# Performance work log

Hardware: AMD Instinct MI355X
Metric: run time of the kernel (lower is better)

The kernel has to match this reference:

```python
import jax, jax.numpy as jnp
import numpy as np

B, U, F = 32768, 256, 256  # batch, units, input features
LR = 0.01                  # inner_lr
EPS = 1e-3                 # TF LayerNormalization default epsilon


def _layer_norm(x, gamma, beta):
    m = jnp.mean(x, axis=-1, keepdims=True)
    v = jnp.var(x, axis=-1, keepdims=True)
    return (x - m) * jax.lax.rsqrt(v + EPS) * gamma + beta


def _enc(W1, b1, W2, b2, u):
    # mlp_2 inner encoder: Dense(4U, gelu-exact) -> Dense(U)
    return jax.nn.gelu(u @ W1 + b1, approximate=False) @ W2 + b2


def setup_inputs() -> dict:
    key = jax.random.key(0)
    ks = jax.random.split(key, 12)
    def w(k, shape):
        fan_in = shape[0]
        return jax.random.normal(k, shape, jnp.float32) / np.sqrt(fan_in)
    return {
        "x": jax.random.normal(ks[0], (B, F), jnp.float32),
        "h_prev": jax.random.normal(ks[1], (B, U), jnp.float32),
        "W_phi": w(ks[2], (F + U, U)), "b_phi": jnp.zeros((U,), jnp.float32),
        "W_psi": w(ks[3], (F + U, U)), "b_psi": jnp.zeros((U,), jnp.float32),
        "W1": w(ks[4], (U, 4 * U)), "b1": jnp.zeros((4 * U,), jnp.float32),
        "W2": w(ks[5], (4 * U, U)), "b2": jnp.zeros((U,), jnp.float32),
        "W_g": w(ks[6], (U, U)), "g_bias": jnp.zeros((U,), jnp.float32),
        "ln_gamma": jnp.ones((U,), jnp.float32), "ln_beta": jnp.zeros((U,), jnp.float32),
        "W_h": w(ks[7], (U, U)), "h_bias": jnp.zeros((U,), jnp.float32),
    }


def reference(x, h_prev, W_phi, b_phi, W_psi, b_psi, W1, b1, W2, b2,
              W_g, g_bias, ln_gamma, ln_beta, W_h, h_bias):
    z = jnp.concatenate([x, h_prev], axis=-1)          # [B, F+U]
    phi = z @ W_phi + b_phi                            # [B, U], also the inner target

    def inner_loss(params):
        W1_, b1_, W2_, b2_ = params
        r = _enc(W1_, b1_, W2_, b2_, phi) @ W_g + g_bias
        r = _layer_norm(r, ln_gamma, ln_beta)
        return jnp.mean(jnp.square(r - phi)), r

    params = (W1, b1, W2, b2)
    # inner_iterations = 1: one SGD step on the inner-encoder weights only
    (_, recon), grads = jax.value_and_grad(inner_loss, has_aux=True)(params)
    params = tuple(p - LR * g for p, g in zip(params, grads))

    psi = z @ W_psi + b_psi                            # [B, U]
    feat = _enc(*params, psi) + 0.1 * recon            # updated encoder on psi
    out = feat @ W_h + h_bias                          # new hidden / cell output
    return out
```

## Files before the change

### kernel.cpp

```cpp
#include <hip/hip_runtime.h>
#include <math.h>

#define B_N 32768
#define U_N 256
#define H_N 1024
#define LR_C 0.01f
#define EPS_C 1e-3f

typedef unsigned short ushort_t;
typedef unsigned int uint_t;
using frag8 = __attribute__((ext_vector_type(8))) short;
using f32x4 = __attribute__((ext_vector_type(4))) float;

__device__ __forceinline__ float erf_fast(float y) {
    float ay = fabsf(y);
    float t = __builtin_amdgcn_rcpf(fmaf(0.3275911f, ay, 1.0f));
    float p = fmaf(1.061405429f, t, -1.453152027f);
    p = fmaf(p, t, 1.421413741f);
    p = fmaf(p, t, -0.284496736f);
    p = fmaf(p, t, 0.254829592f);
    p = p * t;
    float e = __expf(-ay * ay);
    float r = fmaf(-p, e, 1.0f);
    return copysignf(r, y);
}
__device__ __forceinline__ float gelu_f(float x) {
    return 0.5f * x * (1.0f + erf_fast(x * 0.7071067811865475f));
}
__device__ __forceinline__ void gelu_pair(float x, float& g, float& d) {
    float ay = fabsf(x) * 0.7071067811865475f;
    float t = __builtin_amdgcn_rcpf(fmaf(0.3275911f, ay, 1.0f));
    float p = fmaf(1.061405429f, t, -1.453152027f);
    p = fmaf(p, t, 1.421413741f);
    p = fmaf(p, t, -0.284496736f);
    p = fmaf(p, t, 0.254829592f);
    p = p * t;
    float e = __expf(-ay * ay);
    float er = copysignf(fmaf(-p, e, 1.0f), x);
    float c = 0.5f * (1.0f + er);
    g = x * c;
    d = fmaf(x * 0.3989422804014327f, e, c);
}
__device__ __forceinline__ void splitf(float v, ushort_t& h, ushort_t& l) {
    uint_t u = __float_as_uint(v);
    h = (ushort_t)(u >> 16);
    float r = v - __uint_as_float(u & 0xFFFF0000u);
    uint_t ru = __float_as_uint(r);
    l = (ushort_t)((ru + 0x7FFFu + ((ru >> 16) & 1u)) >> 16);
}
__device__ __forceinline__ ushort_t cvt_rne(float v) {
    uint_t u = __float_as_uint(v);
    return (ushort_t)((u + 0x7FFFu + ((u >> 16) & 1u)) >> 16);
}
__device__ __forceinline__ float bf2f(ushort_t u) {
    return __uint_as_float((uint_t)u << 16);
}
__device__ __forceinline__ void unpack2(uint_t pa, uint_t pb, uint_t& hw, uint_t& lw) {
    hw = __builtin_amdgcn_perm(pb, pa, 0x07060302u);
    lw = __builtin_amdgcn_perm(pb, pa, 0x05040100u);
}
__device__ __forceinline__ size_t swz(int n, int k, int K) {
    return (size_t)n * K +
           (size_t)((k & ~31) | ((((k >> 3) & 3) ^ ((n >> 1) & 3)) << 3) | (k & 7));
}
__device__ __forceinline__ void gload16(const ushort_t* g, ushort_t* l) {
    __builtin_amdgcn_global_load_lds(
        (const __attribute__((address_space(1))) void*)g,
        (__attribute__((address_space(3))) void*)l, 16, 0, 0);
}

#define EPI_NONE 0
#define EPI_GELU 1
#define EPI_ADDS 3

#define BEP_P   0
#define BEP_PT  1
#define BEP_A1  2
#define BEP_DAT 3

template<int ACONCAT, int APACK, int EPI, int OPACK>
__global__ __launch_bounds__(256)
void mgemm_k(const float* A, const float* A2, const uint_t* __restrict__ AP,
             const ushort_t* __restrict__ BTh, const ushort_t* __restrict__ BTl,
             const float* __restrict__ bias, const ushort_t* __restrict__ Xr,
             float* C, uint_t* Cp,
             int M, int N, int K)
{
    __shared__ ushort_t Ah[128 * 40], Al[128 * 40];
    __shared__ ushort_t Bh[128 * 32], Bl[128 * 32];
    const int tid = threadIdx.x;
    const int m0 = blockIdx.x * 128, n0 = blockIdx.y * 128;
    const int lane = tid & 63, w = tid >> 6;
    const int wm = (w & 1) * 64, wn = (w >> 1) * 64;
    const int fr = lane & 15, fq = lane >> 4;
    const int sr = tid >> 1;
    const int sk = (tid & 1) * 16;

    f32x4 acc[4][4];
    #pragma unroll
    for (int i = 0; i < 4; i++)
        #pragma unroll
        for (int j = 0; j < 4; j++) acc[i][j] = (f32x4){0.f, 0.f, 0.f, 0.f};

    for (int k0 = 0; k0 < K; k0 += 32) {
        {
            const int r0w = w * 32;
            const size_t so = (size_t)(n0 + r0w + (lane >> 2)) * K + k0 + ((lane & 3) << 3);
            gload16(&BTh[so],                  &Bh[r0w * 32]);
            gload16(&BTh[so + (size_t)16 * K], &Bh[(r0w + 16) * 32]);
            gload16(&BTl[so],                  &Bl[r0w * 32]);
            gload16(&BTl[so + (size_t)16 * K], &Bl[(r0w + 16) * 32]);
        }
        if (APACK) {
            const uint_t* ap = AP + (size_t)(m0 + sr) * K + k0 + sk;
            uint4 p0 = *(const uint4*)(ap);
            uint4 p1 = *(const uint4*)(ap + 4);
            uint4 p2 = *(const uint4*)(ap + 8);
            uint4 p3 = *(const uint4*)(ap + 12);
            uint4 h0, h1, l0, l1;
            unpack2(p0.x, p0.y, h0.x, l0.x); unpack2(p0.z, p0.w, h0.y, l0.y);
            unpack2(p1.x, p1.y, h0.z, l0.z); unpack2(p1.z, p1.w, h0.w, l0.w);
            unpack2(p2.x, p2.y, h1.x, l1.x); unpack2(p2.z, p2.w, h1.y, l1.y);
            unpack2(p3.x, p3.y, h1.z, l1.z); unpack2(p3.z, p3.w, h1.w, l1.w);
            *(uint4*)&Ah[sr * 40 + sk]     = h0;
            *(uint4*)&Ah[sr * 40 + sk + 8] = h1;
            *(uint4*)&Al[sr * 40 + sk]     = l0;
            *(uint4*)&Al[sr * 40 + sk + 8] = l1;
        } else {
            #pragma unroll
            for (int g = 0; g < 2; g++) {
                uint4 qh, qa;
                uint_t ph[4], pl[4];
                #pragma unroll
                for (int c = 0; c < 2; c++) {
                    const int ak = k0 + sk + g * 8 + c * 4;
                    const float* ap;
                    if (ACONCAT) ap = (ak < 256) ? (A + (size_t)(m0 + sr) * 256 + ak)
                                                 : (A2 + (size_t)(m0 + sr) * 256 + (ak - 256));
                    else         ap = A + (size_t)(m0 + sr) * K + ak;
                    float4 v = *(const float4*)ap;
                    ushort_t h0,h1,h2,h3,l0,l1,l2,l3;
                    splitf(v.x,h0,l0); splitf(v.y,h1,l1); splitf(v.z,h2,l2); splitf(v.w,h3,l3);
                    ph[c*2]   = (uint_t)h0 | ((uint_t)h1 << 16);
                    ph[c*2+1] = (uint_t)h2 | ((uint_t)h3 << 16);
                    pl[c*2]   = (uint_t)l0 | ((uint_t)l1 << 16);
                    pl[c*2+1] = (uint_t)l2 | ((uint_t)l3 << 16);
                }
                qh.x = ph[0]; qh.y = ph[1]; qh.z = ph[2]; qh.w = ph[3];
                qa.x = pl[0]; qa.y = pl[1]; qa.z = pl[2]; qa.w = pl[3];
                *(uint4*)&Ah[sr * 40 + sk + g * 8] = qh;
                *(uint4*)&Al[sr * 40 + sk + g * 8] = qa;
            }
        }
        __syncthreads();

        frag8 afh[4], afl[4], bfh[4], bfl[4];
        #pragma unroll
        for (int i = 0; i < 4; i++) {
            const int ar = wm + i * 16 + fr;
            afh[i] = *(frag8*)&Ah[ar * 40 + fq * 8];
            afl[i] = *(frag8*)&Al[ar * 40 + fq * 8];
        }
        #pragma unroll
        for (int j = 0; j < 4; j++) {
            const int br = wn + j * 16 + fr;
            const int bs = br * 32 + ((fq ^ ((br >> 1) & 3)) << 3);
            bfh[j] = *(frag8*)&Bh[bs];
            bfl[j] = *(frag8*)&Bl[bs];
        }
        #pragma unroll
        for (int i = 0; i < 4; i++)
            #pragma unroll
            for (int j = 0; j < 4; j++) {
                acc[i][j] = __builtin_amdgcn_mfma_f32_16x16x32_bf16(afh[i], bfh[j], acc[i][j], 0, 0, 0);
                acc[i][j] = __builtin_amdgcn_mfma_f32_16x16x32_bf16(afh[i], bfl[j], acc[i][j], 0, 0, 0);
                acc[i][j] = __builtin_amdgcn_mfma_f32_16x16x32_bf16(afl[i], bfh[j], acc[i][j], 0, 0, 0);
            }
        __syncthreads();
    }

    float bv[4] = {0.f, 0.f, 0.f, 0.f};
    if (bias != nullptr)
        #pragma unroll
        for (int j = 0; j < 4; j++) bv[j] = bias[n0 + wn + j * 16 + fr];
    #pragma unroll
    for (int i = 0; i < 4; i++)
        #pragma unroll
        for (int j = 0; j < 4; j++) {
            const int col = n0 + wn + j * 16 + fr;
            #pragma unroll
            for (int r = 0; r < 4; r++) {
                const int row = m0 + wm + i * 16 + fq * 4 + r;
                const size_t off = (size_t)row * N + col;
                float c = acc[i][j][r] + bv[j];
                if (EPI == EPI_GELU)      c = gelu_f(c);
                else if (EPI == EPI_ADDS) c = c + 0.1f * bf2f(Xr[off]);
                if (OPACK) {
                    ushort_t h, l;
                    splitf(c, h, l);
                    Cp[off] = ((uint_t)h << 16) | (uint_t)l;
                } else {
                    C[off] = c;
                }
            }
        }
}

template<int ACONCAT, int BEP>
__global__ __launch_bounds__(256)
void bgemm_k(const void* Av, const float* A2f, const ushort_t* __restrict__ BTh,
             const float* __restrict__ bias, const ushort_t* __restrict__ GpIn,
             ushort_t* Crm, ushort_t* Cct, ushort_t* GpOut,
             int M, int N, int K)
{
    __shared__ ushort_t Ah[128 * 40];
    __shared__ ushort_t Bh[128 * 32];
    const int tid = threadIdx.x;
    const int m0 = blockIdx.x * 128, n0 = blockIdx.y * 128;
    const int lane = tid & 63, w = tid >> 6;
    const int wm = (w & 1) * 64, wn = (w >> 1) * 64;
    const int fr = lane & 15, fq = lane >> 4;
    const int sr = tid >> 1;
    const int sk = (tid & 1) * 16;

    f32x4 acc[4][4];
    #pragma unroll
    for (int i = 0; i < 4; i++)
        #pragma unroll
        for (int j = 0; j < 4; j++) acc[i][j] = (f32x4){0.f, 0.f, 0.f, 0.f};

    for (int k0 = 0; k0 < K; k0 += 32) {
        {
            const int r0w = w * 32;
            const size_t so = (size_t)(n0 + r0w + (lane >> 2)) * K + k0 + ((lane & 3) << 3);
            gload16(&BTh[so],                  &Bh[r0w * 32]);
            gload16(&BTh[so + (size_t)16 * K], &Bh[(r0w + 16) * 32]);
        }
        if (ACONCAT) {
            const float* A = (const float*)Av;
            #pragma unroll
            for (int g = 0; g < 2; g++) {
                uint_t ph[4];
                #pragma unroll
                for (int c = 0; c < 2; c++) {
                    const int ak = k0 + sk + g * 8 + c * 4;
                    const float* ap = (ak < 256) ? (A + (size_t)(m0 + sr) * 256 + ak)
                                                 : (A2f + (size_t)(m0 + sr) * 256 + (ak - 256));
                    float4 v = *(const float4*)ap;
                    ph[c*2]   = (uint_t)cvt_rne(v.x) | ((uint_t)cvt_rne(v.y) << 16);
                    ph[c*2+1] = (uint_t)cvt_rne(v.z) | ((uint_t)cvt_rne(v.w) << 16);
                }
                uint4 q; q.x = ph[0]; q.y = ph[1]; q.z = ph[2]; q.w = ph[3];
                *(uint4*)&Ah[sr * 40 + sk + g * 8] = q;
            }
        } else {
            const ushort_t* A = (const ushort_t*)Av;
            const size_t ao = (size_t)(m0 + sr) * K + k0 + sk;
            *(uint4*)&Ah[sr * 40 + sk]     = *(const uint4*)&A[ao];
            *(uint4*)&Ah[sr * 40 + sk + 8] = *(const uint4*)&A[ao + 8];
        }
        __syncthreads();

        frag8 af[4], bf[4];
        #pragma unroll
        for (int i = 0; i < 4; i++) af[i] = *(frag8*)&Ah[(wm + i * 16 + fr) * 40 + fq * 8];
        #pragma unroll
        for (int j = 0; j < 4; j++) {
            const int br = wn + j * 16 + fr;
            bf[j] = *(frag8*)&Bh[br * 32 + ((fq ^ ((br >> 1) & 3)) << 3)];
        }
        #pragma unroll
        for (int i = 0; i < 4; i++)
            #pragma unroll
            for (int j = 0; j < 4; j++)
                acc[i][j] = __builtin_amdgcn_mfma_f32_16x16x32_bf16(af[i], bf[j], acc[i][j], 0, 0, 0);
        __syncthreads();
    }

    float bv[4] = {0.f, 0.f, 0.f, 0.f};
    if (bias != nullptr)
        #pragma unroll
        for (int j = 0; j < 4; j++) bv[j] = bias[n0 + wn + j * 16 + fr];
    #pragma unroll
    for (int i = 0; i < 4; i++)
        #pragma unroll
        for (int j = 0; j < 4; j++) {
            const int col = n0 + wn + j * 16 + fr;
            const int rowb = m0 + wm + i * 16 + fq * 4;
            float v[4];
            #pragma unroll
            for (int r = 0; r < 4; r++) v[r] = acc[i][j][r] + bv[j];
            if (BEP == BEP_A1) {
                ushort_t gc[4];
                #pragma unroll
                for (int r = 0; r < 4; r++) {
                    float g, d;
                    gelu_pair(v[r], g, d);
                    gc[r] = cvt_rne(g);
                    Crm[(size_t)(rowb + r) * N + col] = gc[r];
                    GpOut[(size_t)(rowb + r) * N + col] = cvt_rne(d);
                }
                uint_t p0 = (uint_t)gc[0] | ((uint_t)gc[1] << 16);
                uint_t p1 = (uint_t)gc[2] | ((uint_t)gc[3] << 16);
                *(uint2*)&Cct[(size_t)col * M + rowb] = (uint2){p0, p1};
            } else if (BEP == BEP_DAT) {
                ushort_t dc[4];
                #pragma unroll
                for (int r = 0; r < 4; r++)
                    dc[r] = cvt_rne(v[r] * bf2f(GpIn[(size_t)(rowb + r) * N + col]));
                uint_t p0 = (uint_t)dc[0] | ((uint_t)dc[1] << 16);
                uint_t p1 = (uint_t)dc[2] | ((uint_t)dc[3] << 16);
                *(uint2*)&Cct[(size_t)col * M + rowb] = (uint2){p0, p1};
            } else {
                ushort_t cc[4];
                #pragma unroll
                for (int r = 0; r < 4; r++) {
                    cc[r] = cvt_rne(v[r]);
                    Crm[(size_t)(rowb + r) * N + col] = cc[r];
                }
                if (BEP == BEP_PT) {
                    uint_t p0 = (uint_t)cc[0] | ((uint_t)cc[1] << 16);
                    uint_t p1 = (uint_t)cc[2] | ((uint_t)cc[3] << 16);
                    *(uint2*)&Cct[(size_t)col * M + rowb] = (uint2){p0, p1};
                }
            }
        }
}

__global__ __launch_bounds__(256)
void wgrad_k(const ushort_t* __restrict__ AT, const ushort_t* __restrict__ BTt,
             float* C, int M, int N, int KA, int kofsA, int KB, int kofsB, int KC)
{
    __shared__ ushort_t Ah[128 * 40];
    __shared__ ushort_t Bh[128 * 40];
    const int tid = threadIdx.x;
    const int m0 = blockIdx.x * 128, n0 = blockIdx.y * 128;
    const int kbA = kofsA + blockIdx.z * KC;
    const int kbB = kofsB + blockIdx.z * KC;
    const int lane = tid & 63, w = tid >> 6;
    const int wm = (w & 1) * 64, wn = (w >> 1) * 64;
    const int fr = lane & 15, fq = lane >> 4;
    const int sr = tid >> 1;
    const int sk = (tid & 1) * 16;

    f32x4 acc[4][4];
    #pragma unroll
    for (int i = 0; i < 4; i++)
        #pragma unroll
        for (int j = 0; j < 4; j++) acc[i][j] = (f32x4){0.f, 0.f, 0.f, 0.f};

    for (int k0 = 0; k0 < KC; k0 += 32) {
        const size_t ao = (size_t)(m0 + sr) * KA + kbA + k0 + sk;
        *(uint4*)&Ah[sr * 40 + sk]     = *(const uint4*)&AT[ao];
        *(uint4*)&Ah[sr * 40 + sk + 8] = *(const uint4*)&AT[ao + 8];
        const size_t bo = (size_t)(n0 + sr) * KB + kbB + k0 + sk;
        *(uint4*)&Bh[sr * 40 + sk]     = *(const uint4*)&BTt[bo];
        *(uint4*)&Bh[sr * 40 + sk + 8] = *(const uint4*)&BTt[bo + 8];
        __syncthreads();

        frag8 af[4], bf[4];
        #pragma unroll
        for (int i = 0; i < 4; i++) af[i] = *(frag8*)&Ah[(wm + i * 16 + fr) * 40 + fq * 8];
        #pragma unroll
        for (int j = 0; j < 4; j++) bf[j] = *(frag8*)&Bh[(wn + j * 16 + fr) * 40 + fq * 8];
        #pragma unroll
        for (int i = 0; i < 4; i++)
            #pragma unroll
            for (int j = 0; j < 4; j++)
                acc[i][j] = __builtin_amdgcn_mfma_f32_16x16x32_bf16(af[i], bf[j], acc[i][j], 0, 0, 0);
        __syncthreads();
    }
    #pragma unroll
    for (int i = 0; i < 4; i++)
        #pragma unroll
        for (int j = 0; j < 4; j++) {
            const int col = n0 + wn + j * 16 + fr;
            #pragma unroll
            for (int r = 0; r < 4; r++) {
                const int row = m0 + wm + i * 16 + fq * 4 + r;
                atomicAdd(&C[(size_t)row * N + col], acc[i][j][r]);
            }
        }
}

__global__ __launch_bounds__(256)
void colsumT_k(const ushort_t* __restrict__ T, float* db, int LD, int cols)
{
    const int n = blockIdx.x * 4 + (threadIdx.x >> 6);
    const int lane = threadIdx.x & 63;
    const ushort_t* row = T + (size_t)n * LD;
    float s = 0.f;
    for (int c = lane * 8; c < cols; c += 512) {
        uint4 q = *(const uint4*)&row[c];
        uint_t u[4] = {q.x, q.y, q.z, q.w};
        #pragma unroll
        for (int t = 0; t < 4; t++) {
            s += bf2f((ushort_t)(u[t] & 0xFFFF));
            s += bf2f((ushort_t)(u[t] >> 16));
        }
    }
    #pragma unroll
    for (int o = 32; o > 0; o >>= 1) s += __shfl_xor(s, o);
    if (lane == 0) atomicAdd(&db[n], s);
}

__global__ __launch_bounds__(256)
void ln_bf_k(const ushort_t* r0, const ushort_t* __restrict__ phi,
             const float* __restrict__ gamma, const float* __restrict__ beta,
             ushort_t* recon, ushort_t* dr0)
{
    const int lane = threadIdx.x & 63;
    const int wv = threadIdx.x >> 6;
    const int row = blockIdx.x * 4 + wv;
    const size_t base = (size_t)row * U_N + (lane << 2);

    uint2 xu = *(const uint2*)(r0 + base);
    uint2 pu = *(const uint2*)(phi + base);
    float xs[4] = { bf2f((ushort_t)(xu.x & 0xFFFF)), bf2f((ushort_t)(xu.x >> 16)),
                    bf2f((ushort_t)(xu.y & 0xFFFF)), bf2f((ushort_t)(xu.y >> 16)) };
    float ps[4] = { bf2f((ushort_t)(pu.x & 0xFFFF)), bf2f((ushort_t)(pu.x >> 16)),
                    bf2f((ushort_t)(pu.y & 0xFFFF)), bf2f((ushort_t)(pu.y >> 16)) };
    float s = xs[0] + xs[1] + xs[2] + xs[3];
    float sq = xs[0]*xs[0] + xs[1]*xs[1] + xs[2]*xs[2] + xs[3]*xs[3];
    #pragma unroll
    for (int o = 32; o > 0; o >>= 1) { s += __shfl_xor(s, o); sq += __shfl_xor(sq, o); }
    const float m   = s * (1.0f / U_N);
    const float var = sq * (1.0f / U_N) - m * m;
    const float inv = rsqrtf(var + EPS_C);

    float4 gv = *(const float4*)(gamma + (lane << 2));
    float4 bvv = *(const float4*)(beta + (lane << 2));
    float gs[4] = {gv.x, gv.y, gv.z, gv.w};
    float bs[4] = {bvv.x, bvv.y, bvv.z, bvv.w};
    float rh[4], dh[4], rc[4];
    float s1 = 0.f, s2 = 0.f;
    const float gscale = 2.0f / ((float)B_N * (float)U_N);
    #pragma unroll
    for (int j = 0; j < 4; j++) {
        rh[j] = (xs[j] - m) * inv;
        rc[j] = rh[j] * gs[j] + bs[j];
        float g2 = gscale * (rc[j] - ps[j]);
        dh[j] = g2 * gs[j];
        s1 += dh[j];
        s2 += dh[j] * rh[j];
    }
    #pragma unroll
    for (int o = 32; o > 0; o >>= 1) { s1 += __shfl_xor(s1, o); s2 += __shfl_xor(s2, o); }
    const float mu1 = s1 * (1.0f / U_N);
    const float mu2 = s2 * (1.0f / U_N);
    ushort_t oc[4], dc[4];
    #pragma unroll
    for (int j = 0; j < 4; j++) {
        oc[j] = cvt_rne(rc[j]);
        dc[j] = cvt_rne(inv * (dh[j] - mu1 - rh[j] * mu2));
    }
    *(uint2*)(recon + base) = (uint2){ (uint_t)oc[0] | ((uint_t)oc[1] << 16),
                                       (uint_t)oc[2] | ((uint_t)oc[3] << 16) };
    *(uint2*)(dr0 + base)   = (uint2){ (uint_t)dc[0] | ((uint_t)dc[1] << 16),
                                       (uint_t)dc[2] | ((uint_t)dc[3] << 16) };
}

template<int HASL>
__global__ __launch_bounds__(256)
void tsplit_k(const float* __restrict__ W, ushort_t* __restrict__ Th,
              ushort_t* __restrict__ Tl, int R, int C)
{
    __shared__ float t[64][65];
    const int tid = threadIdx.x;
    const int R0 = blockIdx.x * 64, C0 = blockIdx.y * 64;
    const int c = tid & 63, rb = (tid >> 6) * 16;
    for (int i = 0; i < 16; i++)
        t[rb + i][c] = W[(size_t)(R0 + rb + i) * C + C0 + c];
    __syncthreads();
    const int orr = tid & 63, ob = (tid >> 6) * 16;
    for (int i = 0; i < 16; i++) {
        const int oc = ob + i;
        ushort_t h, l;
        splitf(t[orr][oc], h, l);
        const size_t d = swz(C0 + oc, R0 + orr, R);
        Th[d] = h;
        if (HASL) Tl[d] = l;
    }
}

__global__ __launch_bounds__(256)
void tupd_k(const float* __restrict__ W, const float* __restrict__ dW,
            ushort_t* __restrict__ Th, ushort_t* __restrict__ Tl, int R, int C)
{
    __shared__ float t[64][65];
    const int tid = threadIdx.x;
    const int R0 = blockIdx.x * 64, C0 = blockIdx.y * 64;
    const int c = tid & 63, rb = (tid >> 6) * 16;
    for (int i = 0; i < 16; i++) {
        const size_t o = (size_t)(R0 + rb + i) * C + C0 + c;
        t[rb + i][c] = W[o] - LR_C * dW[o];
    }
    __syncthreads();
    const int orr = tid & 63, ob = (tid >> 6) * 16;
    for (int i = 0; i < 16; i++) {
        const int oc = ob + i;
        ushort_t h, l;
        splitf(t[orr][oc], h, l);
        const size_t d = swz(C0 + oc, R0 + orr, R);
        Th[d] = h;
        Tl[d] = l;
    }
}

__global__ __launch_bounds__(256)
void scvt_k(const float* __restrict__ W, ushort_t* __restrict__ Th, int n4)
{
    const int i = blockIdx.x * 256 + threadIdx.x;
    if (i >= n4) return;
    float4 v = *(const float4*)(W + (size_t)i * 4);
    const int f = i * 4;
    const int row = f >> 8, col = f & 255;
    uint2 ph;
    ph.x = (uint_t)cvt_rne(v.x) | ((uint_t)cvt_rne(v.y) << 16);
    ph.y = (uint_t)cvt_rne(v.z) | ((uint_t)cvt_rne(v.w) << 16);
    *(uint2*)&Th[swz(row, col, 256)] = ph;
}

__global__ __launch_bounds__(256)
void bupd_k(const float* __restrict__ b1, const float* __restrict__ db1,
            const float* __restrict__ b2, const float* __restrict__ db2,
            float* __restrict__ b1u, float* __restrict__ b2u)
{
    const int i = blockIdx.x * 256 + threadIdx.x;
    if (i < H_N) b1u[i] = b1[i] - LR_C * db1[i];
    else if (i < H_N + U_N) b2u[i - H_N] = b2[i - H_N] - LR_C * db2[i - H_N];
}

extern "C" void kernel_launch(void* const* d_in, const int* in_sizes, int n_in,
                              void* d_out, int out_size, void* d_ws, size_t ws_size,
                              hipStream_t stream)
{
    const float* x      = (const float*)d_in[0];
    const float* h_prev = (const float*)d_in[1];
    const float* W_phi  = (const float*)d_in[2];
    const float* b_phi  = (const float*)d_in[3];
    const float* W_psi  = (const float*)d_in[4];
    const float* b_psi  = (const float*)d_in[5];
    const float* W1     = (const float*)d_in[6];
    const float* b1     = (const float*)d_in[7];
    const float* W2     = (const float*)d_in[8];
    const float* b2     = (const float*)d_in[9];
    const float* W_g    = (const float*)d_in[10];
    const float* g_bias = (const float*)d_in[11];
    const float* gamma  = (const float*)d_in[12];
    const float* beta   = (const float*)d_in[13];
    const float* W_h    = (const float*)d_in[14];
    const float* h_bias = (const float*)d_in[15];
    float* out = (float*)d_out;

    const size_t BU = (size_t)B_N * U_N;
    const size_t UH = (size_t)U_N * H_N;

    float* ws  = (float*)d_ws;
    float* dW1 = ws;
    float* db1 = dW1 + UH;
    float* dW2 = db1 + H_N;
    float* db2 = dW2 + UH;
    float* b1u = db2 + U_N;
    float* b2u = b1u + H_N;
    ushort_t* us = (ushort_t*)(((uintptr_t)(b2u + U_N) + 15) & ~(uintptr_t)15);
    ushort_t* WphiT_h = us;
    ushort_t* WpsiT_h = WphiT_h + 131072;     ushort_t* WpsiT_l = WpsiT_h + 131072;
    ushort_t* W1T_h   = WpsiT_l + 131072;
    ushort_t* W2T_h   = W1T_h + 262144;
    ushort_t* W2s_h   = W2T_h + 262144;
    ushort_t* Wgs_h   = W2s_h + 262144;
    ushort_t* WgT_h   = Wgs_h + 65536;
    ushort_t* W1uT_h  = WgT_h + 65536;        ushort_t* W1uT_l = W1uT_h + 262144;
    ushort_t* W2uT_h  = W1uT_l + 262144;      ushort_t* W2uT_l = W2uT_h + 262144;
    ushort_t* WhT_h   = W2uT_l + 262144;      ushort_t* WhT_l  = WhT_h + 65536;
    ushort_t* phi_bf  = WhT_l + 65536;
    ushort_t* phiT_bf = phi_bf + BU;
    ushort_t* recon_bf= phiT_bf + BU;
    ushort_t* chunk0  = recon_bf + BU;
    const size_t P_bytes = (size_t)((char*)chunk0 - (char*)d_ws);

    int GA = 2;
    while (GA < 256 && P_bytes + (size_t)(B_N / GA) * 10240 + (1 << 20) > ws_size) GA *= 2;
    size_t region = (size_t)(B_N / GA) * 10240;
    int GC = 1;
    while (GC < 256) {
        size_t cC = (size_t)(B_N / GC) * 6144;
        size_t r = cC > region ? cC : region;
        if (P_bytes + r + (1 << 20) <= ws_size) { region = r; break; }
        GC *= 2;
    }
    const int BcA = B_N / GA;
    const int BcC = B_N / GC;
    const int KC = (BcA >= 8192) ? 512 : ((BcA >= 1024) ? BcA / 16 : BcA);
    const int Z  = BcA / KC;

    ushort_t* g1  = chunk0;
    ushort_t* gp  = g1  + (size_t)BcA * H_N;
    ushort_t* g1T = gp  + (size_t)BcA * H_N;
    ushort_t* daT = g1T + (size_t)BcA * H_N;
    ushort_t* e_b = daT + (size_t)BcA * H_N;
    ushort_t* r0b = e_b + (size_t)BcA * U_N;
    ushort_t* deb = r0b + (size_t)BcA * U_N;
    ushort_t* deT = deb + (size_t)BcA * U_N;
    uint_t* psi_p  = (uint_t*)chunk0;
    uint_t* h2_p   = psi_p + (size_t)BcC * U_N;
    uint_t* feat_p = h2_p  + (size_t)BcC * H_N;

    hipMemsetAsync(dW1, 0, (2 * UH + H_N + U_N) * sizeof(float), stream);

    dim3 blk(256);
    tsplit_k<0><<<dim3(8, 4),  blk, 0, stream>>>(W_phi, WphiT_h, nullptr, 512, 256);
    tsplit_k<1><<<dim3(8, 4),  blk, 0, stream>>>(W_psi, WpsiT_h, WpsiT_l, 512, 256);
    tsplit_k<0><<<dim3(4, 16), blk, 0, stream>>>(W1, W1T_h, nullptr, 256, 1024);
    tsplit_k<0><<<dim3(16, 4), blk, 0, stream>>>(W2, W2T_h, nullptr, 1024, 256);
    tsplit_k<0><<<dim3(4, 4),  blk, 0, stream>>>(W_g, WgT_h, nullptr, 256, 256);
    tsplit_k<1><<<dim3(4, 4),  blk, 0, stream>>>(W_h, WhT_h, WhT_l, 256, 256);
    scvt_k<<<dim3(256), blk, 0, stream>>>(W2, W2s_h, 65536);
    scvt_k<<<dim3(64),  blk, 0, stream>>>(W_g, Wgs_h, 16384);

    bgemm_k<1, BEP_PT><<<dim3(B_N / 128, 2), blk, 0, stream>>>(
        x, h_prev, WphiT_h, b_phi, nullptr, phi_bf, phiT_bf, nullptr, B_N, U_N, 512);

    for (int c = 0; c < GA; c++) {
        const size_t off = (size_t)c * BcA;
        const ushort_t* phic = phi_bf + off * U_N;
        bgemm_k<0, BEP_A1><<<dim3(BcA / 128, 8), blk, 0, stream>>>(
            phic, nullptr, W1T_h, b1, nullptr, g1, g1T, gp, BcA, H_N, U_N);
        bgemm_k<0, BEP_P><<<dim3(BcA / 128, 2), blk, 0, stream>>>(
            g1, nullptr, W2T_h, b2, nullptr, e_b, nullptr, nullptr, BcA, U_N, H_N);
        bgemm_k<0, BEP_P><<<dim3(BcA / 128, 2), blk, 0, stream>>>(
            e_b, nullptr, WgT_h, g_bias, nullptr, r0b, nullptr, nullptr, BcA, U_N, U_N);
        ln_bf_k<<<dim3(BcA / 4), blk, 0, stream>>>(r0b, phic, gamma, beta,
                                                   recon_bf + off * U_N, r0b);
        bgemm_k<0, BEP_PT><<<dim3(BcA / 128, 2), blk, 0, stream>>>(
            r0b, nullptr, Wgs_h, nullptr, nullptr, deb, deT, nullptr, BcA, U_N, U_N);
        bgemm_k<0, BEP_DAT><<<dim3(BcA / 128, 8), blk, 0, stream>>>(
            deb, nullptr, W2s_h, nullptr, gp, nullptr, daT, nullptr, BcA, H_N, U_N);
        wgrad_k<<<dim3(8, 2, Z), blk, 0, stream>>>(g1T, deT, dW2, H_N, U_N,
                                                   BcA, 0, BcA, 0, KC);
        colsumT_k<<<dim3(U_N / 4), blk, 0, stream>>>(deT, db2, BcA, BcA);
        wgrad_k<<<dim3(2, 8, Z), blk, 0, stream>>>(phiT_bf, daT, dW1, U_N, H_N,
                                                   B_N, (int)off, BcA, 0, KC);
        colsumT_k<<<dim3(H_N / 4), blk, 0, stream>>>(daT, db1, BcA, BcA);
    }

    bupd_k<<<dim3(5), blk, 0, stream>>>(b1, db1, b2, db2, b1u, b2u);
    tupd_k<<<dim3(4, 16), blk, 0, stream>>>(W1, dW1, W1uT_h, W1uT_l, 256, 1024);
    tupd_k<<<dim3(16, 4), blk, 0, stream>>>(W2, dW2, W2uT_h, W2uT_l, 1024, 256);

    for (int c = 0; c < GC; c++) {
        const size_t off = (size_t)c * BcC;
        mgemm_k<1, 0, EPI_NONE, 1><<<dim3(BcC / 128, 2), blk, 0, stream>>>(
            x + off * 256, h_prev + off * U_N, nullptr,
            WpsiT_h, WpsiT_l, b_psi, nullptr,
            nullptr, psi_p, BcC, U_N, 512);
        mgemm_k<0, 1, EPI_GELU, 1><<<dim3(BcC / 128, 8), blk, 0, stream>>>(
            nullptr, nullptr, psi_p,
            W1uT_h, W1uT_l, b1u, nullptr,
            nullptr, h2_p, BcC, H_N, U_N);
        mgemm_k<0, 1, EPI_ADDS, 1><<<dim3(BcC / 128, 2), blk, 0, stream>>>(
            nullptr, nullptr, h2_p,
            W2uT_h, W2uT_l, b2u, recon_bf + off * U_N,
            nullptr, feat_p, BcC, U_N, H_N);
        mgemm_k<0, 1, EPI_NONE, 0><<<dim3(BcC / 128, 2), blk, 0, stream>>>(
            nullptr, nullptr, feat_p,
            WhT_h, WhT_l, h_bias, nullptr,
            out + off * U_N, nullptr, BcC, U_N, U_N);
    }
}
```

Before: 868.4 us.

## Fold W2·W_g into one precomputed matrix and fuse bias-gradient column sums

```diff
diff --git a/kernel.cpp b/kernel.cpp
--- a/kernel.cpp
+++ b/kernel.cpp
@@ -210,7 +210,7 @@
 __global__ __launch_bounds__(256)
 void bgemm_k(const void* Av, const float* A2f, const ushort_t* __restrict__ BTh,
              const float* __restrict__ bias, const ushort_t* __restrict__ GpIn,
-             ushort_t* Crm, ushort_t* Cct, ushort_t* GpOut,
+             ushort_t* Crm, ushort_t* Cct, ushort_t* GpOut, float* dbsum,
              int M, int N, int K)
 {
     __shared__ ushort_t Ah[128 * 40];
@@ -281,6 +281,7 @@
     if (bias != nullptr)
         #pragma unroll
         for (int j = 0; j < 4; j++) bv[j] = bias[n0 + wn + j * 16 + fr];
+    float cs[4] = {0.f, 0.f, 0.f, 0.f};
     #pragma unroll
     for (int i = 0; i < 4; i++)
         #pragma unroll
@@ -306,8 +307,11 @@
             } else if (BEP == BEP_DAT) {
                 ushort_t dc[4];
                 #pragma unroll
-                for (int r = 0; r < 4; r++)
-                    dc[r] = cvt_rne(v[r] * bf2f(GpIn[(size_t)(rowb + r) * N + col]));
+                for (int r = 0; r < 4; r++) {
+                    float pr = v[r] * bf2f(GpIn[(size_t)(rowb + r) * N + col]);
+                    dc[r] = cvt_rne(pr);
+                    cs[j] += pr;
+                }
                 uint_t p0 = (uint_t)dc[0] | ((uint_t)dc[1] << 16);
                 uint_t p1 = (uint_t)dc[2] | ((uint_t)dc[3] << 16);
                 *(uint2*)&Cct[(size_t)col * M + rowb] = (uint2){p0, p1};
@@ -318,6 +322,7 @@
                     cc[r] = cvt_rne(v[r]);
                     Crm[(size_t)(rowb + r) * N + col] = cc[r];
                 }
+                cs[j] += v[0] + v[1] + v[2] + v[3];
                 if (BEP == BEP_PT) {
                     uint_t p0 = (uint_t)cc[0] | ((uint_t)cc[1] << 16);
                     uint_t p1 = (uint_t)cc[2] | ((uint_t)cc[3] << 16);
@@ -325,6 +330,15 @@
                 }
             }
         }
+    if (dbsum != nullptr) {
+        #pragma unroll
+        for (int j = 0; j < 4; j++) {
+            float s = cs[j];
+            s += __shfl_xor(s, 16);
+            s += __shfl_xor(s, 32);
+            if (fq == 0) atomicAdd(&dbsum[n0 + wn + j * 16 + fr], s);
+        }
+    }
 }
 
 __global__ __launch_bounds__(256)
@@ -381,27 +395,6 @@
                 atomicAdd(&C[(size_t)row * N + col], acc[i][j][r]);
             }
         }
-}
-
-__global__ __launch_bounds__(256)
-void colsumT_k(const ushort_t* __restrict__ T, float* db, int LD, int cols)
-{
-    const int n = blockIdx.x * 4 + (threadIdx.x >> 6);
-    const int lane = threadIdx.x & 63;
-    const ushort_t* row = T + (size_t)n * LD;
-    float s = 0.f;
-    for (int c = lane * 8; c < cols; c += 512) {
-        uint4 q = *(const uint4*)&row[c];
-        uint_t u[4] = {q.x, q.y, q.z, q.w};
-        #pragma unroll
-        for (int t = 0; t < 4; t++) {
-            s += bf2f((ushort_t)(u[t] & 0xFFFF));
-            s += bf2f((ushort_t)(u[t] >> 16));
-        }
-    }
-    #pragma unroll
-    for (int o = 32; o > 0; o >>= 1) s += __shfl_xor(s, o);
-    if (lane == 0) atomicAdd(&db[n], s);
 }
 
 __global__ __launch_bounds__(256)
@@ -519,6 +512,28 @@
     ph.x = (uint_t)cvt_rne(v.x) | ((uint_t)cvt_rne(v.y) << 16);
     ph.y = (uint_t)cvt_rne(v.z) | ((uint_t)cvt_rne(v.w) << 16);
     *(uint2*)&Th[swz(row, col, 256)] = ph;
+}
+
+__global__ __launch_bounds__(256)
+void wcmul_k(const float* __restrict__ W2, const float* __restrict__ Wg,
+             float* __restrict__ Wc)
+{
+    const int i = blockIdx.x;
+    const int j = threadIdx.x;
+    float s = 0.f;
+    for (int k = 0; k < 256; k++)
+        s = fmaf(W2[i * 256 + k], Wg[k * 256 + j], s);
+    Wc[i * 256 + j] = s;
+}
+__global__ __launch_bounds__(256)
+void bcmul_k(const float* __restrict__ b2, const float* __restrict__ Wg,
+             const float* __restrict__ gb, float* __restrict__ bc)
+{
+    const int j = threadIdx.x;
+    float s = gb[j];
+    for (int k = 0; k < 256; k++)
+        s = fmaf(b2[k], Wg[k * 256 + j], s);
+    bc[j] = s;
 }
 
 __global__ __launch_bounds__(256)
@@ -563,15 +578,16 @@
     float* db2 = dW2 + UH;
     float* b1u = db2 + U_N;
     float* b2u = b1u + H_N;
-    ushort_t* us = (ushort_t*)(((uintptr_t)(b2u + U_N) + 15) & ~(uintptr_t)15);
+    float* bc  = b2u + U_N;
+    float* Wc  = bc + U_N;
+    ushort_t* us = (ushort_t*)(((uintptr_t)(Wc + UH) + 15) & ~(uintptr_t)15);
     ushort_t* WphiT_h = us;
     ushort_t* WpsiT_h = WphiT_h + 131072;     ushort_t* WpsiT_l = WpsiT_h + 131072;
-    ushort_t* W1T_h   = WpsiT_l + 131072;
-    ushort_t* W2T_h   = W1T_h + 262144;
-    ushort_t* W2s_h   = W2T_h + 262144;
+    ushort_t* WcT_h   = WpsiT_l + 131072;
+    ushort_t* W1T_h   = WcT_h + 262144;
+    ushort_t* W2s_h   = W1T_h + 262144;
     ushort_t* Wgs_h   = W2s_h + 262144;
-    ushort_t* WgT_h   = Wgs_h + 65536;
-    ushort_t* W1uT_h  = WgT_h + 65536;        ushort_t* W1uT_l = W1uT_h + 262144;
+    ushort_t* W1uT_h  = Wgs_h + 65536;        ushort_t* W1uT_l = W1uT_h + 262144;
     ushort_t* W2uT_h  = W1uT_l + 262144;      ushort_t* W2uT_l = W2uT_h + 262144;
     ushort_t* WhT_h   = W2uT_l + 262144;      ushort_t* WhT_l  = WhT_h + 65536;
     ushort_t* phi_bf  = WhT_l + 65536;
@@ -613,36 +629,37 @@
     tsplit_k<0><<<dim3(8, 4),  blk, 0, stream>>>(W_phi, WphiT_h, nullptr, 512, 256);
     tsplit_k<1><<<dim3(8, 4),  blk, 0, stream>>>(W_psi, WpsiT_h, WpsiT_l, 512, 256);
     tsplit_k<0><<<dim3(4, 16), blk, 0, stream>>>(W1, W1T_h, nullptr, 256, 1024);
-    tsplit_k<0><<<dim3(16, 4), blk, 0, stream>>>(W2, W2T_h, nullptr, 1024, 256);
-    tsplit_k<0><<<dim3(4, 4),  blk, 0, stream>>>(W_g, WgT_h, nullptr, 256, 256);
     tsplit_k<1><<<dim3(4, 4),  blk, 0, stream>>>(W_h, WhT_h, WhT_l, 256, 256);
     scvt_k<<<dim3(256), blk, 0, stream>>>(W2, W2s_h, 65536);
     scvt_k<<<dim3(64),  blk, 0, stream>>>(W_g, Wgs_h, 16384);
+    wcmul_k<<<dim3(1024), blk, 0, stream>>>(W2, W_g, Wc);
+    bcmul_k<<<dim3(1), blk, 0, stream>>>(b2, W_g, g_bias, bc);
+    tsplit_k<0><<<dim3(16, 4), blk, 0, stream>>>(Wc, WcT_h, nullptr, 1024, 256);
 
     bgemm_k<1, BEP_PT><<<dim3(B_N / 128, 2), blk, 0, stream>>>(
-        x, h_prev, WphiT_h, b_phi, nullptr, phi_bf, phiT_bf, nullptr, B_N, U_N, 512);
+        x, h_prev, WphiT_h, b_phi, nullptr, phi_bf, phiT_bf, nullptr, nullptr,
+        B_N, U_N, 512);
 
     for (int c = 0; c < GA; c++) {
         const size_t off = (size_t)c * BcA;
         const ushort_t* phic = phi_bf + off * U_N;
         bgemm_k<0, BEP_A1><<<dim3(BcA / 128, 8), blk, 0, stream>>>(
-            phic, nullptr, W1T_h, b1, nullptr, g1, g1T, gp, BcA, H_N, U_N);
+            phic, nullptr, W1T_h, b1, nullptr, g1, g1T, gp, nullptr, BcA, H_N, U_N);
         bgemm_k<0, BEP_P><<<dim3(BcA / 128, 2), blk, 0, stream>>>(
-            g1, nullptr, W2T_h, b2, nullptr, e_b, nullptr, nullptr, BcA, U_N, H_N);
-        bgemm_k<0, BEP_P><<<dim3(BcA / 128, 2), blk, 0, stream>>>(
-            e_b, nullptr, WgT_h, g_bias, nullptr, r0b, nullptr, nullptr, BcA, U_N, U_N);
+            g1, nullptr, WcT_h, bc, nullptr, r0b, nullptr, nullptr, nullptr,
+            BcA, U_N, H_N);
         ln_bf_k<<<dim3(BcA / 4), blk, 0, stream>>>(r0b, phic, gamma, beta,
                                                    recon_bf + off * U_N, r0b);
         bgemm_k<0, BEP_PT><<<dim3(BcA / 128, 2), blk, 0, stream>>>(
-            r0b, nullptr, Wgs_h, nullptr, nullptr, deb, deT, nullptr, BcA, U_N, U_N);
+            r0b, nullptr, Wgs_h, nullptr, nullptr, deb, deT, nullptr, db2,
+            BcA, U_N, U_N);
         bgemm_k<0, BEP_DAT><<<dim3(BcA / 128, 8), blk, 0, stream>>>(
-            deb, nullptr, W2s_h, nullptr, gp, nullptr, daT, nullptr, BcA, H_N, U_N);
+            deb, nullptr, W2s_h, nullptr, gp, nullptr, daT, nullptr, db1,
+            BcA, H_N, U_N);
         wgrad_k<<<dim3(8, 2, Z), blk, 0, stream>>>(g1T, deT, dW2, H_N, U_N,
                                                    BcA, 0, BcA, 0, KC);
-        colsumT_k<<<dim3(U_N / 4), blk, 0, stream>>>(deT, db2, BcA, BcA);
         wgrad_k<<<dim3(2, 8, Z), blk, 0, stream>>>(phiT_bf, daT, dW1, U_N, H_N,
                                                    B_N, (int)off, BcA, 0, KC);
-        colsumT_k<<<dim3(H_N / 4), blk, 0, stream>>>(daT, db1, BcA, BcA);
     }
 
     bupd_k<<<dim3(5), blk, 0, stream>>>(b1, db1, b2, db2, b1u, b2u);
```

New measurement: 845.5 us (median of 2 runs). -2.6%, faster.
